# Kernel optimization log

Hardware: AMD Instinct MI355X
Metric: run time of the kernel (lower is better)

## Reference

```python
import jax, jax.numpy as jnp
import numpy as np

L = 3        # n_hidden_layers
H = 256      # hidden_state_size
K = 20       # n_mixture_components
IN = 2       # INPUT_SIZE (hardcoded in source)
OUT = 5      # OUTPUT_SIZE (hardcoded in source)
B, T = 128, 1000


def lstm_cell(x, h, c, Wih, Whh, bih, bhh):
    # PyTorch LSTMCell: gates ordered (i, f, g, o)
    gates = x @ Wih.T + bih + h @ Whh.T + bhh
    i, f, g, o = jnp.split(gates, 4, axis=-1)
    c2 = jax.nn.sigmoid(f) * c + jax.nn.sigmoid(i) * jnp.tanh(g)
    h2 = jax.nn.sigmoid(o) * jnp.tanh(c2)
    return h2, c2


def setup_inputs() -> dict:
    key = jax.random.key(0)
    ks = jax.random.split(key, 13)
    s = 1.0 / np.sqrt(H)
    u = lambda k, shp: jax.random.uniform(k, shp, jnp.float32, -s, s)
    return {
        "x": jax.random.normal(ks[0], (B, T, IN), jnp.float32),
        "W_ih0": u(ks[1], (4 * H, IN)),
        "W_hh0": u(ks[2], (4 * H, H)),
        "b_ih0": u(ks[3], (4 * H,)),
        "b_hh0": u(ks[4], (4 * H,)),
        "W_ih": u(ks[5], (L - 1, 4 * H, IN + H)),
        "W_hh": u(ks[6], (L - 1, 4 * H, H)),
        "b_ih": u(ks[7], (L - 1, 4 * H)),
        "b_hh": u(ks[8], (L - 1, 4 * H)),
        "Wg": u(ks[9], (OUT * K, IN + H)),
        "bg": u(ks[10], (OUT * K,)),
        "Ww": u(ks[11], (K, IN + H)),
        "bw": u(ks[12], (K,)),
    }


def reference(x, W_ih0, W_hh0, b_ih0, b_hh0, W_ih, W_hh, b_ih, b_hh, Wg, bg, Ww, bw):
    Bn = x.shape[0]
    h0 = jnp.zeros((L, Bn, H), x.dtype)
    c0 = jnp.zeros((L, Bn, H), x.dtype)

    def step(carry, x_t):
        h, c = carry
        hs, cs = [], []
        hh, cc = lstm_cell(x_t, h[0], c[0], W_ih0, W_hh0, b_ih0, b_hh0)
        hs.append(hh); cs.append(cc)
        for i in range(L - 1):  # small static layer count
            xi = jnp.concatenate([x_t, hh], axis=1)  # skip connection
            hh, cc = lstm_cell(xi, h[i + 1], c[i + 1], W_ih[i], W_hh[i], b_ih[i], b_hh[i])
            hs.append(hh); cs.append(cc)
        x_n = jnp.concatenate([x_t, hh], axis=1)           # [B, 2+H]
        g = x_n @ Wg.T + bg                                 # [B, 5K]
        w = jax.nn.softmax(x_n @ Ww.T + bw, axis=-1)        # [B, K]
        return (jnp.stack(hs), jnp.stack(cs)), (g, w)

    _, (gs, ws) = jax.lax.scan(step, (h0, c0), jnp.swapaxes(x, 0, 1))
    # scan stacked along time -> [T, B, .]; transpose to [B, T, .]
    return jnp.swapaxes(gs, 0, 1), jnp.swapaxes(ws, 0, 1)
```

## Files before the change

### kernel.cpp

```cpp
#include <hip/hip_runtime.h>
#include <hip/hip_fp16.h>
#include <stdint.h>

#define T_STEPS 1000
#define G4      1024
#define NOUT    100
#define NW      20
#define NTHM    512
#define NGROUPS 8
#define NROLE   12
#define BT      16

constexpr int    OFF_HBUF  = 0;
constexpr int    OFF_CNT   = OFF_HBUF + NGROUPS*3*4*16*128;
constexpr int    OFF_HEADW = OFF_CNT + NGROUPS*448;
constexpr int    OFF_HXB   = OFF_HEADW + 120*132;
constexpr int    OFF_MISC  = OFF_HXB + 360;
constexpr int    OFF_WREG  = OFF_MISC + NROLE*768;
constexpr size_t WS_DW     = (size_t)OFF_WREG + (size_t)NROLE*32*512*4;
constexpr size_t GOFF      = (size_t)128*1000*100;

__device__ __forceinline__ float sigf(float x)     { return 1.0f / (1.0f + __expf(-x)); }
__device__ __forceinline__ float tanhfast(float x) { return 2.0f / (1.0f + __expf(-2.0f * x)) - 1.0f; }

typedef _Float16 h2v    __attribute__((ext_vector_type(2)));
typedef _Float16 f16x8v __attribute__((ext_vector_type(8)));
typedef float    f32x4v __attribute__((ext_vector_type(4)));
#define MFMA16(A, B, C) __builtin_amdgcn_mfma_f32_16x16x32_f16((A), (B), (C), 0, 0, 0)

__device__ __forceinline__ float dot2f(uint32_t w, uint32_t h, float acc) {
    return __builtin_amdgcn_fdot2(__builtin_bit_cast(h2v, w),
                                  __builtin_bit_cast(h2v, h), acc, false);
}
__device__ __forceinline__ uint32_t pk(float a, float b) {
    __half2 h = __floats2half2_rn(a, b);
    return *reinterpret_cast<uint32_t*>(&h);
}

__device__ __forceinline__ void role_params(int rw, int& stage, int& idx, int& U, int& u0) {
    stage = rw >> 2; idx = rw & 3; U = 64; u0 = 64*idx;
}

__device__ __forceinline__ uint32_t fetch_wdw(int rw, int tid, int slot, int d,
                                              const float* __restrict__ Whh0,
                                              const float* __restrict__ WihL,
                                              const float* __restrict__ WhhL) {
    int stage, idx, U, u0; role_params(rw, stage, idx, U, u0);
    int wave = tid >> 6, lane = tid & 63;
    int ntl = slot >> 4, kt = slot & 15;
    int nt = 2*wave + ntl;
    if (stage == 0 && kt >= 8) return 0u;
    int gate = nt >> 2, usub = nt & 3;
    int j = gate*256 + u0 + usub*16 + (lane & 15);
    int khalf = lane >> 4;
    if (stage == 0) {
        int k = kt*32 + khalf*8 + 2*d;
        return pk(Whh0[(size_t)j*256 + k], Whh0[(size_t)j*256 + k + 1]);
    }
    if (kt < 8) {
        int k = kt*32 + khalf*8 + 2*d;
        const float* Wi = WihL + (size_t)(stage-1)*G4*258;
        return pk(Wi[(size_t)j*258 + 2 + k], Wi[(size_t)j*258 + 3 + k]);
    }
    int k = (kt-8)*32 + khalf*8 + 2*d;
    const float* Wh = WhhL + (size_t)(stage-1)*G4*256;
    return pk(Wh[(size_t)j*256 + k], Wh[(size_t)j*256 + k + 1]);
}

__global__ void pack_wreg(const float* __restrict__ Whh0, const float* __restrict__ WihL,
                          const float* __restrict__ WhhL, uint32_t* __restrict__ wsd) {
    int slot = blockIdx.x & 31, rw = blockIdx.x >> 5;
    int tid = threadIdx.x;
    uint32_t* dst = wsd + OFF_WREG + ((size_t)(rw*32 + slot)*512 + tid)*4;
    dst[0] = fetch_wdw(rw, tid, slot, 0, Whh0, WihL, WhhL);
    dst[1] = fetch_wdw(rw, tid, slot, 1, Whh0, WihL, WhhL);
    dst[2] = fetch_wdw(rw, tid, slot, 2, Whh0, WihL, WhhL);
    dst[3] = fetch_wdw(rw, tid, slot, 3, Whh0, WihL, WhhL);
}

__global__ void pack_misc(const float* __restrict__ Wih0,
                          const float* __restrict__ bih0, const float* __restrict__ bhh0,
                          const float* __restrict__ WihL,
                          const float* __restrict__ bihL, const float* __restrict__ bhhL,
                          uint32_t* __restrict__ wsd) {
    int id = blockIdx.x * blockDim.x + threadIdx.x;
    if (id >= NROLE*768) return;
    int rw = id / 768, i = id % 768;
    int qq = i / 256, rem = i % 256, gate = rem / 64, u = rem % 64;
    int stage, idx, U, u0; role_params(rw, stage, idx, U, u0);
    int j = gate*256 + u0 + u;
    float v;
    if (stage == 0)      v = (qq == 0) ? bih0[j] + bhh0[j] : Wih0[j*2 + (qq-1)];
    else if (stage == 1) v = (qq == 0) ? bihL[j] + bhhL[j] : WihL[(size_t)j*258 + (qq-1)];
    else                 v = (qq == 0) ? bihL[G4+j] + bhhL[G4+j]
                                       : WihL[(size_t)G4*258 + (size_t)j*258 + (qq-1)];
    ((float*)wsd)[OFF_MISC + id] = v;
}

__global__ void pack_head(const float* __restrict__ Wg, const float* __restrict__ bg,
                          const float* __restrict__ Ww, const float* __restrict__ bw,
                          uint32_t* __restrict__ wsd) {
    int id = blockIdx.x * blockDim.x + threadIdx.x;
    if (id < 120*132) {
        int jo = id / 132, d = id % 132;
        uint32_t v = 0;
        if (d < 128) {
            int k = 2*d;
            const float* row = (jo < 100) ? (Wg + (size_t)jo*258) : (Ww + (size_t)(jo-100)*258);
            v = pk(row[2+k], row[3+k]);
        }
        wsd[OFF_HEADW + id] = v;
    } else if (id < 120*132 + 360) {
        int p = id - 120*132, jo = p/3, qq = p%3;
        const float* row = (jo < 100) ? (Wg + (size_t)jo*258) : (Ww + (size_t)(jo-100)*258);
        float v = (qq == 0) ? ((jo < 100) ? bg[jo] : bw[jo-100]) : row[qq-1];
        ((float*)wsd)[OFF_HXB + p] = v;
    }
}

__global__ void zero_cnt(uint32_t* __restrict__ wsd) {
    int id = blockIdx.x * blockDim.x + threadIdx.x;
    if (id < NGROUPS*448) wsd[OFF_CNT + id] = 0;
}

__device__ __forceinline__ void pollCnt(uint32_t* c, uint32_t tgt) {
    int spins = 0;
    while (__hip_atomic_load(c, __ATOMIC_RELAXED, __HIP_MEMORY_SCOPE_AGENT) < tgt) {
        __builtin_amdgcn_s_sleep(1);
        if (++spins > (1 << 24)) break;
    }
}
__device__ __forceinline__ void bump(uint32_t* c) {
    __hip_atomic_fetch_add(c, 1u, __ATOMIC_RELAXED, __HIP_MEMORY_SCOPE_AGENT);
}
#define PCC(L) (cnt + (L)*16)

template<int SO>
__device__ __forceinline__ void mfma8(f32x4v& ac0, f32x4v& ac1, const f16x8v (&wrf)[32],
                                      const uint32_t* hb, int rA, int khalf) {
#pragma unroll
    for (int kt = 0; kt < 8; ++kt) {
        uint4 hv = *(const uint4*)(hb + rA*132 + kt*16 + khalf*4);
        f16x8v a = __builtin_bit_cast(f16x8v, hv);
        ac0 = MFMA16(a, wrf[SO + kt], ac0);
        ac1 = MFMA16(a, wrf[16 + SO + kt], ac1);
    }
}

#define READH(BUF, L, SLOT)                                                        \
    { _Pragma("unroll")                                                            \
      for (int p_ = 0; p_ < 2; ++p_) {                                             \
        int idx_ = tid + p_*512;                                                   \
        int r_ = idx_ >> 6, i_ = idx_ & 63;                                        \
        uint64_t v_ = __hip_atomic_load(hbuf64 + (((L)*4 + (SLOT))*16 + r_)*64 + i_, \
                                        __ATOMIC_RELAXED, __HIP_MEMORY_SCOPE_AGENT); \
        *(uint64_t*)&h_lds[BUF][r_][2*i_] = v_;                                    \
      } }

#define DWRITE()                                                                   \
    { _Pragma("unroll")                                                            \
      for (int rg = 0; rg < 4; ++rg) g_s[m0 + rg][gate0][ul0] = ac0[rg];           \
      _Pragma("unroll")                                                            \
      for (int rg = 0; rg < 4; ++rg) g_s[m0 + rg][gate1][ul1] = ac1[rg]; }

#define UPDATE_PASS(PASS, CST, LYR, SLOT)                                          \
    { int r_ = tid & 15, u_ = (PASS)*32 + (tid >> 4);                              \
      float x0 = x_cur[r_][0], x1 = x_cur[r_][1];                                  \
      float gi = g_s[r_][0][u_] + misc_s[0][0][u_] + x0*misc_s[1][0][u_] + x1*misc_s[2][0][u_]; \
      float gf = g_s[r_][1][u_] + misc_s[0][1][u_] + x0*misc_s[1][1][u_] + x1*misc_s[2][1][u_]; \
      float gg = g_s[r_][2][u_] + misc_s[0][2][u_] + x0*misc_s[1][2][u_] + x1*misc_s[2][2][u_]; \
      float go = g_s[r_][3][u_] + misc_s[0][3][u_] + x0*misc_s[1][3][u_] + x1*misc_s[2][3][u_]; \
      float cc_ = sigf(gf)*(CST) + sigf(gi)*tanhfast(gg);                          \
      float hval = sigf(go)*tanhfast(cc_);  (CST) = cc_;                           \
      float h1_ = __shfl_down(hval, 16), h2_ = __shfl_down(hval, 32), h3_ = __shfl_down(hval, 48); \
      if ((tid & 63) < 16) {                                                       \
          uint64_t pv = (uint64_t)pk(hval, h1_) | ((uint64_t)pk(h2_, h3_) << 32);  \
          __hip_atomic_store(hbuf64 + (((LYR)*4 + (SLOT))*16 + r_)*64              \
                                 + (u0 >> 2) + (PASS)*8 + (tid >> 6), pv,          \
                             __ATOMIC_RELAXED, __HIP_MEMORY_SCOPE_AGENT);          \
      } }

#define HEAD_COMPUTE(TT, SLH)                                                      \
    { int jol = tid >> 4, rr2 = tid & 15;                                          \
      float acch = 0.0f;                                                           \
      if (jol < 30) {                                                              \
          _Pragma("unroll")                                                        \
          for (int d4 = 0; d4 < 32; ++d4) {                                        \
              uint4 wv = *(const uint4*)&headw_s[jol*132 + d4*4];                  \
              uint4 hv = *(const uint4*)&h_lds[1][rr2][d4*4];                      \
              acch = dot2f(wv.x, hv.x, acch); acch = dot2f(wv.y, hv.y, acch);      \
              acch = dot2f(wv.z, hv.z, acch); acch = dot2f(wv.w, hv.w, acch);      \
          }                                                                        \
          int jo = idx*30 + jol;                                                   \
          float xa = x_ring[SLH][rr2][0], xb = x_ring[SLH][rr2][1];                \
          acch += hxb_s[jol*3] + xa*hxb_s[jol*3+1] + xb*hxb_s[jol*3+2];            \
          if (jo < NOUT) out[((size_t)(b0 + rr2)*T_STEPS + (TT))*NOUT + jo] = acch; \
          else           wl_s[rr2][jo - NOUT] = acch;                              \
      }                                                                            \
      __syncthreads();                                                             \
      if (idx == 3 && tid < 16) {                                                  \
          int r = tid;                                                             \
          float mx = -1e30f;                                                       \
          _Pragma("unroll")                                                        \
          for (int m = 0; m < NW; ++m) mx = fmaxf(mx, wl_s[r][m]);                 \
          float ss = 0.0f, ee[NW];                                                 \
          _Pragma("unroll")                                                        \
          for (int m = 0; m < NW; ++m) { ee[m] = __expf(wl_s[r][m] - mx); ss += ee[m]; } \
          float inv = 1.0f / ss;                                                   \
          size_t bo = GOFF + ((size_t)(b0 + r)*T_STEPS + (TT))*NW;                 \
          _Pragma("unroll")                                                        \
          for (int m = 0; m < NW; ++m) out[bo + m] = ee[m]*inv;                    \
      } }

template <bool WSPACK>
__global__ __launch_bounds__(NTHM, 1)
void lstm_pipe(const float* __restrict__ x, uint32_t* __restrict__ wsd,
               float* __restrict__ out,
               const float* __restrict__ Whh0, const float* __restrict__ WihL,
               const float* __restrict__ WhhL) {
    __shared__ __align__(16) uint32_t h_lds[2][16][132];
    __shared__ float    g_s[16][4][65];
    __shared__ float    misc_s[3][4][64];
    __shared__ float    x_cur[16][2];
    __shared__ float    x_ring[4][16][2];
    __shared__ __align__(16) uint32_t headw_s[30*132];
    __shared__ float    hxb_s[90];
    __shared__ float    wl_s[16][NW];

    const int tid = threadIdx.x;
    const int bid = blockIdx.x;
    const int g  = bid & (NGROUPS - 1);
    const int rw = bid >> 3;
    int stage, idx, U, u0; role_params(rw, stage, idx, U, u0);
    const int b0 = g * BT;
    const int wave = tid >> 6, lane = tid & 63;
    const int rA = lane & 15, khalf = lane >> 4;
    const int m0 = khalf * 4;
    const int nt0 = 2*wave, nt1 = 2*wave + 1;
    const int gate0 = nt0 >> 2, ul0 = (nt0 & 3)*16 + rA;
    const int gate1 = nt1 >> 2, ul1 = (nt1 & 3)*16 + rA;

    uint64_t* hbuf64 = (uint64_t*)(wsd + OFF_HBUF) + (size_t)g * 12288;
    uint32_t* cnt = wsd + OFF_CNT + g * 448;
    const float* wsf = (const float*)wsd;

    f16x8v wrf[32];
    if (WSPACK) {
#pragma unroll
        for (int s = 0; s < 32; ++s) {
            uint4 v = *(const uint4*)(wsd + OFF_WREG + ((size_t)(rw*32 + s)*512 + tid)*4);
            wrf[s] = __builtin_bit_cast(f16x8v, v);
        }
    } else {
#pragma unroll
        for (int s = 0; s < 32; ++s) {
            uint4 v;
            v.x = fetch_wdw(rw, tid, s, 0, Whh0, WihL, WhhL);
            v.y = fetch_wdw(rw, tid, s, 1, Whh0, WihL, WhhL);
            v.z = fetch_wdw(rw, tid, s, 2, Whh0, WihL, WhhL);
            v.w = fetch_wdw(rw, tid, s, 3, Whh0, WihL, WhhL);
            wrf[s] = __builtin_bit_cast(f16x8v, v);
        }
    }

    for (int i = tid; i < 2*16*132; i += NTHM) (&h_lds[0][0][0])[i] = 0u;
    for (int i = tid; i < 768;      i += NTHM) (&misc_s[0][0][0])[i] = wsf[OFF_MISC + rw*768 + i];
    if (stage == 0) {
        for (int i = tid; i < 30*132; i += NTHM) headw_s[i] = wsd[OFF_HEADW + idx*30*132 + i];
        for (int i = tid; i < 90;     i += NTHM) hxb_s[i]   = wsf[OFF_HXB + idx*90 + i];
    }
    float c_st0 = 0.0f, c_st1 = 0.0f;
    __syncthreads();

    const f32x4v zf4 = {0.0f, 0.0f, 0.0f, 0.0f};

    if (stage == 0) {
        for (int t = 0; t <= 1002; ++t) {
            const bool doL0 = (t < T_STEPS);
            const bool doHd = (t >= 3);
            const int th = t - 3;
            const int sl = t & 3, slp = (t - 1) & 3, slh = th & 3;
            float xv = 0.0f;
            if (doL0 && tid < 32)
                xv = x[((size_t)(b0 + (tid >> 1))*T_STEPS + t)*2 + (tid & 1)];
            if (tid == 0 && doL0 && t >= 1) pollCnt(PCC(0), 4u*(uint32_t)t);
            __syncthreads();
            if (doL0 && t >= 1) READH(0, 0, slp)
            if (doL0 && tid < 32) {
                x_cur[tid >> 1][tid & 1] = xv;
                x_ring[sl][tid >> 1][tid & 1] = xv;
            }
            __syncthreads();
            if (doL0) {
                f32x4v ac0 = zf4, ac1 = zf4;
                mfma8<0>(ac0, ac1, wrf, &h_lds[0][0][0], rA, khalf);
                DWRITE()
            }
            __syncthreads();
            if (doL0) {
                UPDATE_PASS(0, c_st0, 0, sl)
                UPDATE_PASS(1, c_st1, 0, sl)
            }
            __syncthreads();
            if (tid == 0 && doL0) bump(PCC(0));
            if (doHd) {
                if (tid == 0) pollCnt(PCC(2), 4u*(uint32_t)(t - 2));
                __syncthreads();
                READH(1, 2, slh)
                __syncthreads();
                HEAD_COMPUTE(th, slh)
            }
        }
    } else {
        const int OWN_L = stage, IN_L = stage - 1;
        for (int t = 0; t < T_STEPS; ++t) {
            const int sl = t & 3, slp = (t - 1) & 3;
            float xv = 0.0f;
            if (tid < 32)
                xv = x[((size_t)(b0 + (tid >> 1))*T_STEPS + t)*2 + (tid & 1)];
            if (tid == 0) {
                if (t >= 1) pollCnt(PCC(OWN_L), 4u*(uint32_t)t);
                pollCnt(PCC(IN_L), 4u*(uint32_t)(t + 1));
            }
            __syncthreads();
            READH(0, IN_L, sl)
            if (t >= 1) READH(1, OWN_L, slp)
            if (tid < 32) x_cur[tid >> 1][tid & 1] = xv;
            __syncthreads();
            f32x4v ac0 = zf4, ac1 = zf4;
            mfma8<0>(ac0, ac1, wrf, &h_lds[0][0][0], rA, khalf);
            mfma8<8>(ac0, ac1, wrf, &h_lds[1][0][0], rA, khalf);
            DWRITE()
            __syncthreads();
            UPDATE_PASS(0, c_st0, OWN_L, sl)
            UPDATE_PASS(1, c_st1, OWN_L, sl)
            __syncthreads();
            if (tid == 0) bump(PCC(OWN_L));
        }
    }
}

extern "C" void kernel_launch(void* const* d_in, const int* in_sizes, int n_in,
                              void* d_out, int out_size, void* d_ws, size_t ws_size,
                              hipStream_t stream) {
    const float* x    = (const float*)d_in[0];
    const float* Wih0 = (const float*)d_in[1];
    const float* Whh0 = (const float*)d_in[2];
    const float* bih0 = (const float*)d_in[3];
    const float* bhh0 = (const float*)d_in[4];
    const float* WihL = (const float*)d_in[5];
    const float* WhhL = (const float*)d_in[6];
    const float* bihL = (const float*)d_in[7];
    const float* bhhL = (const float*)d_in[8];
    const float* Wg   = (const float*)d_in[9];
    const float* bg   = (const float*)d_in[10];
    const float* Ww   = (const float*)d_in[11];
    const float* bw   = (const float*)d_in[12];
    float*    out = (float*)d_out;
    uint32_t* wsd = (uint32_t*)d_ws;
    (void)in_sizes; (void)n_in; (void)out_size;

    const bool wspack = ws_size >= WS_DW * 4;

    zero_cnt<<<14, 256, 0, stream>>>(wsd);
    pack_misc<<<36, 256, 0, stream>>>(Wih0, bih0, bhh0, WihL, bihL, bhhL, wsd);
    pack_head<<<64, 256, 0, stream>>>(Wg, bg, Ww, bw, wsd);
    if (wspack)
        pack_wreg<<<NROLE*32, 512, 0, stream>>>(Whh0, WihL, WhhL, wsd);

    dim3 grid(NGROUPS * NROLE), block(NTHM);
    void* args[] = {(void*)&x, (void*)&wsd, (void*)&out,
                    (void*)&Whh0, (void*)&WihL, (void*)&WhhL};
    if (wspack) {
        hipError_t err = hipLaunchCooperativeKernel((const void*)lstm_pipe<true>,
                                                    grid, block, args, 0, stream);
        if (err != hipSuccess)
            lstm_pipe<true><<<grid, block, 0, stream>>>(x, wsd, out, Whh0, WihL, WhhL);
    } else {
        hipError_t err = hipLaunchCooperativeKernel((const void*)lstm_pipe<false>,
                                                    grid, block, args, 0, stream);
        if (err != hipSuccess)
            lstm_pipe<false><<<grid, block, 0, stream>>>(x, wsd, out, Whh0, WihL, WhhL);
    }
}
```

Measured before the change: 3.943 ms.

## Replace counter-based inter-block handoff with per-word tagged hidden-state flags

Removes the shared per-layer arrival counters with their thread-0 polling and __syncthreads barriers. Each 64-bit hidden-state word now carries a timestep tag in its upper half, and every reader spins on its own words until the expected tag appears. This drops one block barrier per step and lets consumers start as soon as their data lands, instead of waiting for all producers to bump a counter. The cost is a buffer twice as large that must be zeroed each launch, twice as many global loads per read, and per-thread spinning. x_cur is double-buffered by step parity so the next step can write it while the current update still reads it.

```diff
diff --git a/kernel.cpp b/kernel.cpp
--- a/kernel.cpp
+++ b/kernel.cpp
@@ -12,8 +12,8 @@
 #define BT      16
 
 constexpr int    OFF_HBUF  = 0;
-constexpr int    OFF_CNT   = OFF_HBUF + NGROUPS*3*4*16*128;
-constexpr int    OFF_HEADW = OFF_CNT + NGROUPS*448;
+constexpr int    HBUF_DW   = NGROUPS*3*4*16*256;
+constexpr int    OFF_HEADW = HBUF_DW;
 constexpr int    OFF_HXB   = OFF_HEADW + 120*132;
 constexpr int    OFF_MISC  = OFF_HXB + 360;
 constexpr int    OFF_WREG  = OFF_MISC + NROLE*768;
@@ -118,22 +118,22 @@
     }
 }
 
-__global__ void zero_cnt(uint32_t* __restrict__ wsd) {
+__global__ void zero_hbuf(uint32_t* __restrict__ wsd) {
     int id = blockIdx.x * blockDim.x + threadIdx.x;
-    if (id < NGROUPS*448) wsd[OFF_CNT + id] = 0;
-}
-
-__device__ __forceinline__ void pollCnt(uint32_t* c, uint32_t tgt) {
-    int spins = 0;
-    while (__hip_atomic_load(c, __ATOMIC_RELAXED, __HIP_MEMORY_SCOPE_AGENT) < tgt) {
-        __builtin_amdgcn_s_sleep(1);
-        if (++spins > (1 << 24)) break;
-    }
-}
-__device__ __forceinline__ void bump(uint32_t* c) {
-    __hip_atomic_fetch_add(c, 1u, __ATOMIC_RELAXED, __HIP_MEMORY_SCOPE_AGENT);
-}
-#define PCC(L) (cnt + (L)*16)
+    if (id < HBUF_DW) wsd[OFF_HBUF + id] = 0;
+}
+
+#define READH_TAG(BUF, L, SLOT, WANT)                                              \
+    { _Pragma("unroll")                                                            \
+      for (int p_ = 0; p_ < 4; ++p_) {                                             \
+        int idx_ = tid + p_*512;                                                   \
+        int r_ = idx_ >> 7, c_ = idx_ & 127;                                       \
+        uint64_t* ap_ = hbuf64 + (((L)*4 + (SLOT))*16 + r_)*128 + c_;              \
+        uint64_t v_; int sp_ = 0;                                                  \
+        do { v_ = __hip_atomic_load(ap_, __ATOMIC_RELAXED, __HIP_MEMORY_SCOPE_AGENT); \
+        } while ((uint32_t)(v_ >> 32) != (uint32_t)(WANT) && ++sp_ < (1 << 20));   \
+        h_lds[BUF][r_][c_] = (uint32_t)v_;                                         \
+      } }
 
 template<int SO>
 __device__ __forceinline__ void mfma8(f32x4v& ac0, f32x4v& ac1, const f16x8v (&wrf)[32],
@@ -147,38 +147,32 @@
     }
 }
 
-#define READH(BUF, L, SLOT)                                                        \
-    { _Pragma("unroll")                                                            \
-      for (int p_ = 0; p_ < 2; ++p_) {                                             \
-        int idx_ = tid + p_*512;                                                   \
-        int r_ = idx_ >> 6, i_ = idx_ & 63;                                        \
-        uint64_t v_ = __hip_atomic_load(hbuf64 + (((L)*4 + (SLOT))*16 + r_)*64 + i_, \
-                                        __ATOMIC_RELAXED, __HIP_MEMORY_SCOPE_AGENT); \
-        *(uint64_t*)&h_lds[BUF][r_][2*i_] = v_;                                    \
-      } }
-
 #define DWRITE()                                                                   \
     { _Pragma("unroll")                                                            \
       for (int rg = 0; rg < 4; ++rg) g_s[m0 + rg][gate0][ul0] = ac0[rg];           \
       _Pragma("unroll")                                                            \
       for (int rg = 0; rg < 4; ++rg) g_s[m0 + rg][gate1][ul1] = ac1[rg]; }
 
-#define UPDATE_PASS(PASS, CST, LYR, SLOT)                                          \
-    { int r_ = tid & 15, u_ = (PASS)*32 + (tid >> 4);                              \
-      float x0 = x_cur[r_][0], x1 = x_cur[r_][1];                                  \
-      float gi = g_s[r_][0][u_] + misc_s[0][0][u_] + x0*misc_s[1][0][u_] + x1*misc_s[2][0][u_]; \
-      float gf = g_s[r_][1][u_] + misc_s[0][1][u_] + x0*misc_s[1][1][u_] + x1*misc_s[2][1][u_]; \
-      float gg = g_s[r_][2][u_] + misc_s[0][2][u_] + x0*misc_s[1][2][u_] + x1*misc_s[2][2][u_]; \
-      float go = g_s[r_][3][u_] + misc_s[0][3][u_] + x0*misc_s[1][3][u_] + x1*misc_s[2][3][u_]; \
-      float cc_ = sigf(gf)*(CST) + sigf(gi)*tanhfast(gg);                          \
-      float hval = sigf(go)*tanhfast(cc_);  (CST) = cc_;                           \
-      float h1_ = __shfl_down(hval, 16), h2_ = __shfl_down(hval, 32), h3_ = __shfl_down(hval, 48); \
-      if ((tid & 63) < 16) {                                                       \
-          uint64_t pv = (uint64_t)pk(hval, h1_) | ((uint64_t)pk(h2_, h3_) << 32);  \
-          __hip_atomic_store(hbuf64 + (((LYR)*4 + (SLOT))*16 + r_)*64              \
-                                 + (u0 >> 2) + (PASS)*8 + (tid >> 6), pv,          \
-                             __ATOMIC_RELAXED, __HIP_MEMORY_SCOPE_AGENT);          \
-      } }
+#define UPDATE_STORE(LYR, SLOT, TAG)                                               \
+    { int r_ = tid & 15, up_ = tid >> 4;                                           \
+      int ua_ = 2*up_, ub_ = ua_ + 1;                                              \
+      float x0 = x_cur[par][r_][0], x1 = x_cur[par][r_][1];                        \
+      float gia = g_s[r_][0][ua_] + misc_s[0][0][ua_] + x0*misc_s[1][0][ua_] + x1*misc_s[2][0][ua_]; \
+      float gfa = g_s[r_][1][ua_] + misc_s[0][1][ua_] + x0*misc_s[1][1][ua_] + x1*misc_s[2][1][ua_]; \
+      float gga = g_s[r_][2][ua_] + misc_s[0][2][ua_] + x0*misc_s[1][2][ua_] + x1*misc_s[2][2][ua_]; \
+      float goa = g_s[r_][3][ua_] + misc_s[0][3][ua_] + x0*misc_s[1][3][ua_] + x1*misc_s[2][3][ua_]; \
+      float gib = g_s[r_][0][ub_] + misc_s[0][0][ub_] + x0*misc_s[1][0][ub_] + x1*misc_s[2][0][ub_]; \
+      float gfb = g_s[r_][1][ub_] + misc_s[0][1][ub_] + x0*misc_s[1][1][ub_] + x1*misc_s[2][1][ub_]; \
+      float ggb = g_s[r_][2][ub_] + misc_s[0][2][ub_] + x0*misc_s[1][2][ub_] + x1*misc_s[2][2][ub_]; \
+      float gob = g_s[r_][3][ub_] + misc_s[0][3][ub_] + x0*misc_s[1][3][ub_] + x1*misc_s[2][3][ub_]; \
+      float cca = sigf(gfa)*c_st0 + sigf(gia)*tanhfast(gga);                       \
+      float ha_ = sigf(goa)*tanhfast(cca);  c_st0 = cca;                           \
+      float ccb = sigf(gfb)*c_st1 + sigf(gib)*tanhfast(ggb);                       \
+      float hb_ = sigf(gob)*tanhfast(ccb);  c_st1 = ccb;                           \
+      uint64_t pv = ((uint64_t)(uint32_t)(TAG) << 32) | (uint64_t)pk(ha_, hb_);    \
+      __hip_atomic_store(hbuf64 + (((LYR)*4 + (SLOT))*16 + r_)*128 + idx*32 + up_, \
+                         pv, __ATOMIC_RELAXED, __HIP_MEMORY_SCOPE_AGENT);          \
+      }
 
 #define HEAD_COMPUTE(TT, SLH)                                                      \
     { int jol = tid >> 4, rr2 = tid & 15;                                          \
@@ -221,7 +215,7 @@
     __shared__ __align__(16) uint32_t h_lds[2][16][132];
     __shared__ float    g_s[16][4][65];
     __shared__ float    misc_s[3][4][64];
-    __shared__ float    x_cur[16][2];
+    __shared__ float    x_cur[2][16][2];
     __shared__ float    x_ring[4][16][2];
     __shared__ __align__(16) uint32_t headw_s[30*132];
     __shared__ float    hxb_s[90];
@@ -240,8 +234,7 @@
     const int gate0 = nt0 >> 2, ul0 = (nt0 & 3)*16 + rA;
     const int gate1 = nt1 >> 2, ul1 = (nt1 & 3)*16 + rA;
 
-    uint64_t* hbuf64 = (uint64_t*)(wsd + OFF_HBUF) + (size_t)g * 12288;
-    uint32_t* cnt = wsd + OFF_CNT + g * 448;
+    uint64_t* hbuf64 = (uint64_t*)(wsd + OFF_HBUF) + (size_t)g * 24576;
     const float* wsf = (const float*)wsd;
 
     f16x8v wrf[32];
@@ -279,16 +272,17 @@
             const bool doL0 = (t < T_STEPS);
             const bool doHd = (t >= 3);
             const int th = t - 3;
+            const int par = t & 1;
             const int sl = t & 3, slp = (t - 1) & 3, slh = th & 3;
-            float xv = 0.0f;
-            if (doL0 && tid < 32)
-                xv = x[((size_t)(b0 + (tid >> 1))*T_STEPS + t)*2 + (tid & 1)];
-            if (tid == 0 && doL0 && t >= 1) pollCnt(PCC(0), 4u*(uint32_t)t);
-            __syncthreads();
-            if (doL0 && t >= 1) READH(0, 0, slp)
-            if (doL0 && tid < 32) {
-                x_cur[tid >> 1][tid & 1] = xv;
-                x_ring[sl][tid >> 1][tid & 1] = xv;
+            if (doL0) {
+                float xv = 0.0f;
+                if (tid < 32)
+                    xv = x[((size_t)(b0 + (tid >> 1))*T_STEPS + t)*2 + (tid & 1)];
+                if (t >= 1) READH_TAG(0, 0, slp, t)
+                if (tid < 32) {
+                    x_cur[par][tid >> 1][tid & 1] = xv;
+                    x_ring[sl][tid >> 1][tid & 1] = xv;
+                }
             }
             __syncthreads();
             if (doL0) {
@@ -297,16 +291,9 @@
                 DWRITE()
             }
             __syncthreads();
-            if (doL0) {
-                UPDATE_PASS(0, c_st0, 0, sl)
-                UPDATE_PASS(1, c_st1, 0, sl)
-            }
-            __syncthreads();
-            if (tid == 0 && doL0) bump(PCC(0));
+            if (doL0) UPDATE_STORE(0, sl, t + 1)
             if (doHd) {
-                if (tid == 0) pollCnt(PCC(2), 4u*(uint32_t)(t - 2));
-                __syncthreads();
-                READH(1, 2, slh)
+                READH_TAG(1, 2, slh, th + 1)
                 __syncthreads();
                 HEAD_COMPUTE(th, slh)
             }
@@ -314,28 +301,21 @@
     } else {
         const int OWN_L = stage, IN_L = stage - 1;
         for (int t = 0; t < T_STEPS; ++t) {
+            const int par = t & 1;
             const int sl = t & 3, slp = (t - 1) & 3;
             float xv = 0.0f;
             if (tid < 32)
                 xv = x[((size_t)(b0 + (tid >> 1))*T_STEPS + t)*2 + (tid & 1)];
-            if (tid == 0) {
-                if (t >= 1) pollCnt(PCC(OWN_L), 4u*(uint32_t)t);
-                pollCnt(PCC(IN_L), 4u*(uint32_t)(t + 1));
-            }
-            __syncthreads();
-            READH(0, IN_L, sl)
-            if (t >= 1) READH(1, OWN_L, slp)
-            if (tid < 32) x_cur[tid >> 1][tid & 1] = xv;
+            if (t >= 1) READH_TAG(1, OWN_L, slp, t)
+            READH_TAG(0, IN_L, sl, t + 1)
+            if (tid < 32) x_cur[par][tid >> 1][tid & 1] = xv;
             __syncthreads();
             f32x4v ac0 = zf4, ac1 = zf4;
             mfma8<0>(ac0, ac1, wrf, &h_lds[0][0][0], rA, khalf);
             mfma8<8>(ac0, ac1, wrf, &h_lds[1][0][0], rA, khalf);
             DWRITE()
             __syncthreads();
-            UPDATE_PASS(0, c_st0, OWN_L, sl)
-            UPDATE_PASS(1, c_st1, OWN_L, sl)
-            __syncthreads();
-            if (tid == 0) bump(PCC(OWN_L));
+            UPDATE_STORE(OWN_L, sl, t + 1)
         }
     }
 }
@@ -362,7 +342,7 @@
 
     const bool wspack = ws_size >= WS_DW * 4;
 
-    zero_cnt<<<14, 256, 0, stream>>>(wsd);
+    zero_hbuf<<<768, 512, 0, stream>>>(wsd);
     pack_misc<<<36, 256, 0, stream>>>(Wih0, bih0, bhh0, WihL, bihL, bhhL, wsd);
     pack_head<<<64, 256, 0, stream>>>(Wg, bg, Ww, bw, wsd);
     if (wspack)
```

Result: slower. 4.638 ms (+17.6%).
